# Performance work log

Measured on AMD Instinct MI355X. Metric: run time of the kernel, lower is better.

## Reference

```python
import jax, jax.numpy as jnp
import numpy as np

N = 100000   # nodes
E = 1600000  # edges
IN, HID, OUT = 128, 128, 64
K = 32       # MaxK top-k
NUM_LAYERS = 2


def _xavier(key, shape):
    lim = float(np.sqrt(6.0 / (shape[0] + shape[1])))
    return jax.random.uniform(key, shape, jnp.float32, -lim, lim)


def setup_inputs() -> dict:
    key = jax.random.key(0)
    ks = jax.random.split(key, 8)
    return {
        "x": jax.random.normal(ks[0], (N, IN), jnp.float32),
        "src": jax.random.randint(ks[1], (E,), 0, N, dtype=jnp.int32),
        "dst": jax.random.randint(ks[2], (E,), 0, N, dtype=jnp.int32),
        "W_in": _xavier(ks[3], (IN, HID)), "b_in": jnp.zeros((HID,), jnp.float32),
        "W1": _xavier(ks[4], (HID, HID)), "b1": jnp.zeros((HID,), jnp.float32),
        "bg1": jnp.zeros((HID,), jnp.float32),
        "W2": _xavier(ks[5], (HID, HID)), "b2": jnp.zeros((HID,), jnp.float32),
        "bg2": jnp.zeros((HID,), jnp.float32),
        "W_out": _xavier(ks[6], (HID, OUT)), "b_out": jnp.zeros((OUT,), jnp.float32),
    }


def _maxk(x, k):
    # keep top-k entries per row, zero the rest (straight-through mask)
    _, idx = jax.lax.top_k(x, k)                      # [N, k]
    rows = jnp.arange(x.shape[0])[:, None]
    mask = jnp.zeros_like(x).at[rows, idx].set(1.0)
    return x * mask


def _graph_conv(x, src, dst, bias):
    # DGL GraphConv, norm='both', weight=None: D_dst^{-1/2} A D_src^{-1/2} x + b
    ones = jnp.ones((src.shape[0],), x.dtype)
    deg_out = jnp.maximum(jax.ops.segment_sum(ones, src, num_segments=N), 1.0)
    deg_in = jnp.maximum(jax.ops.segment_sum(ones, dst, num_segments=N), 1.0)
    msg = (x * (deg_out ** -0.5)[:, None])[src]        # [E, HID] gather
    agg = jax.ops.segment_sum(msg, dst, num_segments=N)  # [N, HID] scatter-add
    return agg * (deg_in ** -0.5)[:, None] + bias


def reference(x, src, dst, W_in, b_in, W1, b1, bg1, W2, b2, bg2, W_out, b_out):
    h = jax.nn.relu(x @ W_in + b_in)
    for W, b, bg in ((W1, b1, bg1), (W2, b2, bg2)):
        h = h @ W + b
        h = _maxk(h, K)
        # dropout: eval-mode identity
        h = _graph_conv(h, src, dst, bg)
    return h @ W_out + b_out
```

## Files before the change

kernel.cpp:

```cpp
#include <hip/hip_runtime.h>

#define NN   100000
#define EE   1600000
#define HIDF 128
#define OUTF 64
#define KSEL 32
#define BSH  3
#define NBK  (NN >> BSH)
#define CAPSH 8
#define CAP  (1 << CAPSH)

static __device__ __forceinline__ unsigned int sortable_key(float f) {
    unsigned int u = __float_as_uint(f);
    return (u & 0x80000000u) ? ~u : (u | 0x80000000u);
}

__global__ __launch_bounds__(256) void bin_fill(const int* __restrict__ src,
                                                const int* __restrict__ dst,
                                                int* __restrict__ bcnt,
                                                int* __restrict__ scnt,
                                                int2* __restrict__ bin, int e) {
    int i = blockIdx.x * 256 + threadIdx.x;
    if (i < e) {
        int s = src[i];
        int d = dst[i];
        int b = d >> BSH;
        int pos = atomicAdd(&bcnt[b], 1);
        if (pos < CAP) bin[((size_t)b << CAPSH) + pos] = make_int2(s, d);
        atomicAdd(&scnt[s], 1);
    }
}

__global__ __launch_bounds__(128) void csr_from_bin(const int2* __restrict__ bin,
                                                    const int* __restrict__ bcnt,
                                                    int* __restrict__ row_off,
                                                    int* __restrict__ cnt_in,
                                                    float* __restrict__ dvin,
                                                    int* __restrict__ csr, int n) {
    __shared__ int cnt8[1 << BSH];
    __shared__ int cur8[1 << BSH];
    const int b = blockIdx.x;
    const int t = threadIdx.x;
    if (t < (1 << BSH)) cnt8[t] = 0;
    __syncthreads();
    const int m = min(bcnt[b], CAP);
    const size_t base = (size_t)b << CAPSH;
    for (int e = t; e < m; e += 128) {
        atomicAdd(&cnt8[bin[base + e].y & ((1 << BSH) - 1)], 1);
    }
    __syncthreads();
    if (t < (1 << BSH)) {
        int pre = 0;
#pragma unroll
        for (int q = 0; q < (1 << BSH); ++q) pre += (q < t) ? cnt8[q] : 0;
        int node = (b << BSH) + t;
        int start = (int)base + pre;
        if (node < n) {
            row_off[node] = start;
            cnt_in[node] = cnt8[t];
            dvin[node] = rsqrtf((float)max(cnt8[t], 1));
        }
        cur8[t] = start;
    }
    __syncthreads();
    for (int e = t; e < m; e += 128) {
        int2 r = bin[base + e];
        int pos = atomicAdd(&cur8[r.y & ((1 << BSH) - 1)], 1);
        csr[pos] = r.x;
    }
}

__global__ __launch_bounds__(256) void dvout_pass(const int* __restrict__ scnt,
                                                  float* __restrict__ dvo, int n) {
    int i = blockIdx.x * 256 + threadIdx.x;
    if (i < n) dvo[i] = rsqrtf((float)max(scnt[i], 1));
}

__global__ __launch_bounds__(256, 2) void gemm_relu(const float* __restrict__ A,
                                                    const float* __restrict__ W,
                                                    const float* __restrict__ bias,
                                                    float* __restrict__ out, int n) {
    __shared__ float As[64][128];
    __shared__ float Ws[16][128];
    const int tid = threadIdx.x;
    const int rbase = blockIdx.x * 64;
    const int cc = tid & 31;
    const int r0 = (tid >> 5) * 8;
    float acc[8][4];
#pragma unroll
    for (int i = 0; i < 8; ++i) { acc[i][0] = 0.f; acc[i][1] = 0.f; acc[i][2] = 0.f; acc[i][3] = 0.f; }

    float4 wreg0 = *(const float4*)(W + (size_t)tid * 4);
    float4 wreg1 = *(const float4*)(W + (size_t)(tid + 256) * 4);

#pragma unroll
    for (int q = 0; q < 8; ++q) {
        int f = q * 256 + tid;
        int row = rbase + (f >> 5);
        float4 v = make_float4(0.f, 0.f, 0.f, 0.f);
        if (row < n) v = *(const float4*)(A + (size_t)row * 128 + (f & 31) * 4);
        *(float4*)&As[f >> 5][(f & 31) * 4] = v;
    }

    for (int p = 0; p < 8; ++p) {
        const int kb = p * 16;
        if (p) __syncthreads();
        *(float4*)&Ws[tid >> 5][(tid & 31) * 4] = wreg0;
        *(float4*)&Ws[(tid >> 5) + 8][(tid & 31) * 4] = wreg1;
        if (p < 7) {
            const float* wp = W + (size_t)(kb + 16) * 128;
            wreg0 = *(const float4*)(wp + (size_t)tid * 4);
            wreg1 = *(const float4*)(wp + (size_t)(tid + 256) * 4);
        }
        __syncthreads();
#pragma unroll
        for (int kq = 0; kq < 4; ++kq) {
            int k = kq * 4;
            float4 w0 = *(float4*)&Ws[k + 0][cc * 4];
            float4 w1 = *(float4*)&Ws[k + 1][cc * 4];
            float4 w2 = *(float4*)&Ws[k + 2][cc * 4];
            float4 w3 = *(float4*)&Ws[k + 3][cc * 4];
#pragma unroll
            for (int i = 0; i < 8; ++i) {
                float4 a = *(float4*)&As[r0 + i][kb + k];
                acc[i][0] += a.x * w0.x + a.y * w1.x + a.z * w2.x + a.w * w3.x;
                acc[i][1] += a.x * w0.y + a.y * w1.y + a.z * w2.y + a.w * w3.y;
                acc[i][2] += a.x * w0.z + a.y * w1.z + a.z * w2.z + a.w * w3.z;
                acc[i][3] += a.x * w0.w + a.y * w1.w + a.z * w2.w + a.w * w3.w;
            }
        }
    }
    float4 b4 = *(const float4*)(bias + cc * 4);
#pragma unroll
    for (int i = 0; i < 8; ++i) {
        int gr = rbase + r0 + i;
        if (gr < n) {
            float4 o = make_float4(fmaxf(acc[i][0] + b4.x, 0.f), fmaxf(acc[i][1] + b4.y, 0.f),
                                   fmaxf(acc[i][2] + b4.z, 0.f), fmaxf(acc[i][3] + b4.w, 0.f));
            *(float4*)(out + (size_t)gr * 128 + cc * 4) = o;
        }
    }
}

__global__ __launch_bounds__(256, 2) void gemm_maxk(const float* __restrict__ A,
                                                    const float* __restrict__ W,
                                                    const float* __restrict__ bias,
                                                    const float* __restrict__ dvout,
                                                    float* __restrict__ svals, int n) {
    __shared__ float As[64][128];
    __shared__ float Ws[16][128];
    const int tid = threadIdx.x;
    const int rbase = blockIdx.x * 64;
    const int cc = tid & 31;
    const int r0 = (tid >> 5) * 8;
    float acc[8][4];
#pragma unroll
    for (int i = 0; i < 8; ++i) { acc[i][0] = 0.f; acc[i][1] = 0.f; acc[i][2] = 0.f; acc[i][3] = 0.f; }

    float4 wreg0 = *(const float4*)(W + (size_t)tid * 4);
    float4 wreg1 = *(const float4*)(W + (size_t)(tid + 256) * 4);

#pragma unroll
    for (int q = 0; q < 8; ++q) {
        int f = q * 256 + tid;
        *(float4*)&As[f >> 5][(f & 31) * 4] =
            *(const float4*)(A + (size_t)rbase * 128 + (size_t)f * 4);
    }

    for (int p = 0; p < 8; ++p) {
        const int kb = p * 16;
        if (p) __syncthreads();
        *(float4*)&Ws[tid >> 5][(tid & 31) * 4] = wreg0;
        *(float4*)&Ws[(tid >> 5) + 8][(tid & 31) * 4] = wreg1;
        if (p < 7) {
            const float* wp = W + (size_t)(kb + 16) * 128;
            wreg0 = *(const float4*)(wp + (size_t)tid * 4);
            wreg1 = *(const float4*)(wp + (size_t)(tid + 256) * 4);
        }
        __syncthreads();
#pragma unroll
        for (int kq = 0; kq < 4; ++kq) {
            int k = kq * 4;
            float4 w0 = *(float4*)&Ws[k + 0][cc * 4];
            float4 w1 = *(float4*)&Ws[k + 1][cc * 4];
            float4 w2 = *(float4*)&Ws[k + 2][cc * 4];
            float4 w3 = *(float4*)&Ws[k + 3][cc * 4];
#pragma unroll
            for (int i = 0; i < 8; ++i) {
                float4 a = *(float4*)&As[r0 + i][kb + k];
                acc[i][0] += a.x * w0.x + a.y * w1.x + a.z * w2.x + a.w * w3.x;
                acc[i][1] += a.x * w0.y + a.y * w1.y + a.z * w2.y + a.w * w3.y;
                acc[i][2] += a.x * w0.z + a.y * w1.z + a.z * w2.z + a.w * w3.z;
                acc[i][3] += a.x * w0.w + a.y * w1.w + a.z * w2.w + a.w * w3.w;
            }
        }
    }

    const int lane = tid & 63;
    const int wvi = tid >> 6;
    const bool up = lane >= 32;
    const unsigned lt32 = (1u << (lane & 31)) - 1u;
    float4 b4 = *(const float4*)(bias + cc * 4);

    unsigned keys[8][4];
#pragma unroll
    for (int i = 0; i < 8; ++i) {
        acc[i][0] += b4.x; acc[i][1] += b4.y; acc[i][2] += b4.z; acc[i][3] += b4.w;
        keys[i][0] = sortable_key(acc[i][0]);
        keys[i][1] = sortable_key(acc[i][1]);
        keys[i][2] = sortable_key(acc[i][2]);
        keys[i][3] = sortable_key(acc[i][3]);
    }
    unsigned prefL[8], prefU[8];
#pragma unroll
    for (int i = 0; i < 8; ++i) { prefL[i] = 0u; prefU[i] = 0u; }

    for (int bit = 31; bit >= 8; --bit) {
        unsigned msk = 1u << bit;
#pragma unroll
        for (int i = 0; i < 8; ++i) {
            unsigned cL = prefL[i] | msk;
            unsigned cU = prefU[i] | msk;
            unsigned myc = up ? cU : cL;
            unsigned long long b0 = __ballot(keys[i][0] >= myc);
            unsigned long long b1 = __ballot(keys[i][1] >= myc);
            unsigned long long b2 = __ballot(keys[i][2] >= myc);
            unsigned long long b3 = __ballot(keys[i][3] >= myc);
            int cntL = __popc((unsigned)b0) + __popc((unsigned)b1) +
                       __popc((unsigned)b2) + __popc((unsigned)b3);
            int cntU = __popc((unsigned)(b0 >> 32)) + __popc((unsigned)(b1 >> 32)) +
                       __popc((unsigned)(b2 >> 32)) + __popc((unsigned)(b3 >> 32));
            prefL[i] = (cntL >= KSEL) ? cL : prefL[i];
            prefU[i] = (cntU >= KSEL) ? cU : prefU[i];
        }
    }

#pragma unroll 1
    for (int i = 0; i < 8; ++i) {
        int row = rbase + 16 * wvi + i + (up ? 8 : 0);
        unsigned myp = up ? prefU[i] : prefL[i];
        unsigned kb0 = keys[i][0] & 0xFFFFFF00u, kb1 = keys[i][1] & 0xFFFFFF00u;
        unsigned kb2 = keys[i][2] & 0xFFFFFF00u, kb3 = keys[i][3] & 0xFFFFFF00u;
        unsigned long long g0 = __ballot(kb0 > myp), g1 = __ballot(kb1 > myp);
        unsigned long long g2 = __ballot(kb2 > myp), g3 = __ballot(kb3 > myp);
        unsigned long long e0 = __ballot(kb0 == myp), e1 = __ballot(kb1 == myp);
        unsigned long long e2 = __ballot(kb2 == myp), e3 = __ballot(kb3 == myp);
        unsigned gh0 = up ? (unsigned)(g0 >> 32) : (unsigned)g0;
        unsigned gh1 = up ? (unsigned)(g1 >> 32) : (unsigned)g1;
        unsigned gh2 = up ? (unsigned)(g2 >> 32) : (unsigned)g2;
        unsigned gh3 = up ? (unsigned)(g3 >> 32) : (unsigned)g3;
        unsigned eh0 = up ? (unsigned)(e0 >> 32) : (unsigned)e0;
        unsigned eh1 = up ? (unsigned)(e1 >> 32) : (unsigned)e1;
        unsigned eh2 = up ? (unsigned)(e2 >> 32) : (unsigned)e2;
        unsigned eh3 = up ? (unsigned)(e3 >> 32) : (unsigned)e3;
        int m = __popc(gh0) + __popc(gh1) + __popc(gh2) + __popc(gh3);
        int need = KSEL - m;
        int gpos = __popc(gh0 & lt32) + __popc(gh1 & lt32) + __popc(gh2 & lt32) + __popc(gh3 & lt32);
        int epos = __popc(eh0 & lt32) + __popc(eh1 & lt32) + __popc(eh2 & lt32) + __popc(eh3 & lt32);
        bool ok = row < n;
        float ds = dvout[row];
        size_t base = (size_t)row * 32;
        unsigned cbit = (unsigned)(lane & 31);
        {
            int slot = -1;
            if (kb0 > myp) slot = gpos;
            else if (kb0 == myp && epos < need) slot = m + epos;
            if (slot >= 0 && ok) {
                unsigned u = (__float_as_uint(acc[i][0] * ds) & 0xFFFFFF80u) | (unsigned)(cc * 4 + 0);
                svals[base + slot] = __uint_as_float(u);
            }
            gpos += (gh0 >> cbit) & 1u;
            epos += (eh0 >> cbit) & 1u;
        }
        {
            int slot = -1;
            if (kb1 > myp) slot = gpos;
            else if (kb1 == myp && epos < need) slot = m + epos;
            if (slot >= 0 && ok) {
                unsigned u = (__float_as_uint(acc[i][1] * ds) & 0xFFFFFF80u) | (unsigned)(cc * 4 + 1);
                svals[base + slot] = __uint_as_float(u);
            }
            gpos += (gh1 >> cbit) & 1u;
            epos += (eh1 >> cbit) & 1u;
        }
        {
            int slot = -1;
            if (kb2 > myp) slot = gpos;
            else if (kb2 == myp && epos < need) slot = m + epos;
            if (slot >= 0 && ok) {
                unsigned u = (__float_as_uint(acc[i][2] * ds) & 0xFFFFFF80u) | (unsigned)(cc * 4 + 2);
                svals[base + slot] = __uint_as_float(u);
            }
            gpos += (gh2 >> cbit) & 1u;
            epos += (eh2 >> cbit) & 1u;
        }
        {
            int slot = -1;
            if (kb3 > myp) slot = gpos;
            else if (kb3 == myp && epos < need) slot = m + epos;
            if (slot >= 0 && ok) {
                unsigned u = (__float_as_uint(acc[i][3] * ds) & 0xFFFFFF80u) | (unsigned)(cc * 4 + 3);
                svals[base + slot] = __uint_as_float(u);
            }
        }
    }
}

__global__ __launch_bounds__(256) void agg_kernel(const float* __restrict__ svals,
                                                  const int* __restrict__ row_off,
                                                  const int* __restrict__ cnt_in,
                                                  const int* __restrict__ csr_src,
                                                  const float* __restrict__ dvin,
                                                  const float* __restrict__ bg,
                                                  float* __restrict__ out, int n) {
    __shared__ float acc[4][2][128];
    const int wv = threadIdx.x >> 6;
    const int lane = threadIdx.x & 63;
    const int sub = lane >> 5;
    const int j = lane & 31;
    const int node = blockIdx.x * 4 + wv;
    float* base0 = &acc[wv][0][0];
    base0[lane] = 0.f;
    base0[lane + 64] = 0.f;
    base0[lane + 128] = 0.f;
    base0[lane + 192] = 0.f;
    if (node < n) {
        int s0 = row_off[node], s1 = s0 + cnt_in[node];
        float* Ac = &acc[wv][sub][0];
        int e = s0 + sub;
        for (; e + 2 < s1; e += 4) {
            int sA = csr_src[e];
            int sB = csr_src[e + 2];
            float vA = svals[(size_t)sA * 32 + j];
            float vB = svals[(size_t)sB * 32 + j];
            int fA = (int)(__float_as_uint(vA) & 127u);
            Ac[fA] += vA;
            int fB = (int)(__float_as_uint(vB) & 127u);
            Ac[fB] += vB;
        }
        for (; e < s1; e += 2) {
            int sA = csr_src[e];
            float vA = svals[(size_t)sA * 32 + j];
            int fA = (int)(__float_as_uint(vA) & 127u);
            Ac[fA] += vA;
        }
    }
    if (node < n) {
        float dv = dvin[node];
        float r0 = acc[wv][0][lane] + acc[wv][1][lane];
        float r1 = acc[wv][0][lane + 64] + acc[wv][1][lane + 64];
        out[(size_t)node * 128 + lane] = r0 * dv + bg[lane];
        out[(size_t)node * 128 + lane + 64] = r1 * dv + bg[lane + 64];
    }
}

__global__ __launch_bounds__(256, 2) void gemm_out64(const float* __restrict__ A,
                                                     const float* __restrict__ W,
                                                     const float* __restrict__ bias,
                                                     float* __restrict__ out, int n) {
    __shared__ float As[64][128];
    __shared__ float Ws[32][64];
    const int tid = threadIdx.x;
    const int rbase = blockIdx.x * 64;
    const int cc = tid & 15;
    const int r0 = (tid >> 4) * 4;
    float acc[4][4];
#pragma unroll
    for (int i = 0; i < 4; ++i) { acc[i][0] = 0.f; acc[i][1] = 0.f; acc[i][2] = 0.f; acc[i][3] = 0.f; }

    float4 wreg0 = *(const float4*)(W + (size_t)tid * 4);
    float4 wreg1 = *(const float4*)(W + (size_t)(tid + 256) * 4);

#pragma unroll
    for (int q = 0; q < 8; ++q) {
        int f = q * 256 + tid;
        *(float4*)&As[f >> 5][(f & 31) * 4] =
            *(const float4*)(A + (size_t)rbase * 128 + (size_t)f * 4);
    }

    for (int p = 0; p < 4; ++p) {
        const int kb = p * 32;
        if (p) __syncthreads();
        *(float4*)&Ws[tid >> 4][(tid & 15) * 4] = wreg0;
        *(float4*)&Ws[(tid >> 4) + 16][(tid & 15) * 4] = wreg1;
        if (p < 3) {
            const float* wp = W + (size_t)(kb + 32) * 64;
            wreg0 = *(const float4*)(wp + (size_t)tid * 4);
            wreg1 = *(const float4*)(wp + (size_t)(tid + 256) * 4);
        }
        __syncthreads();
#pragma unroll
        for (int kq = 0; kq < 8; ++kq) {
            int k = kq * 4;
            float4 w0 = *(float4*)&Ws[k + 0][cc * 4];
            float4 w1 = *(float4*)&Ws[k + 1][cc * 4];
            float4 w2 = *(float4*)&Ws[k + 2][cc * 4];
            float4 w3 = *(float4*)&Ws[k + 3][cc * 4];
#pragma unroll
            for (int i = 0; i < 4; ++i) {
                float4 a = *(float4*)&As[r0 + i][kb + k];
                acc[i][0] += a.x * w0.x + a.y * w1.x + a.z * w2.x + a.w * w3.x;
                acc[i][1] += a.x * w0.y + a.y * w1.y + a.z * w2.y + a.w * w3.y;
                acc[i][2] += a.x * w0.z + a.y * w1.z + a.z * w2.z + a.w * w3.z;
                acc[i][3] += a.x * w0.w + a.y * w1.w + a.z * w2.w + a.w * w3.w;
            }
        }
    }
    float4 b4 = *(const float4*)(bias + cc * 4);
#pragma unroll
    for (int i = 0; i < 4; ++i) {
        int gr = rbase + r0 + i;
        if (gr < n) {
            float4 o = make_float4(acc[i][0] + b4.x, acc[i][1] + b4.y,
                                   acc[i][2] + b4.z, acc[i][3] + b4.w);
            *(float4*)(out + (size_t)gr * 64 + cc * 4) = o;
        }
    }
}

extern "C" void kernel_launch(void* const* d_in, const int* in_sizes, int n_in,
                              void* d_out, int out_size, void* d_ws, size_t ws_size,
                              hipStream_t stream) {
    const float* x     = (const float*)d_in[0];
    const int*   src   = (const int*)d_in[1];
    const int*   dst   = (const int*)d_in[2];
    const float* W_in  = (const float*)d_in[3];
    const float* b_in  = (const float*)d_in[4];
    const float* W1    = (const float*)d_in[5];
    const float* b1    = (const float*)d_in[6];
    const float* bg1   = (const float*)d_in[7];
    const float* W2    = (const float*)d_in[8];
    const float* b2    = (const float*)d_in[9];
    const float* bg2   = (const float*)d_in[10];
    const float* W_out = (const float*)d_in[11];
    const float* b_out = (const float*)d_in[12];
    float* out = (float*)d_out;

    char* p = (char*)d_ws;
    auto carve = [&](size_t bytes) {
        char* r = p;
        p += (bytes + 255) & ~(size_t)255;
        return r;
    };
    int*   scnt    = (int*)carve((size_t)NN * 4);
    int*   bcnt    = (int*)carve((size_t)NBK * 4);
    float* dvout   = (float*)carve((size_t)(NN + 128) * 4);
    float* dvin    = (float*)carve((size_t)NN * 4);
    int*   row_off = (int*)carve((size_t)NN * 4);
    int*   cnt_in  = (int*)carve((size_t)NN * 4);
    int*   csr_src = (int*)carve((size_t)NBK * CAP * 4);
    float* hbuf    = (float*)carve((size_t)(NN + 128) * HIDF * 4);
    float* svals   = (float*)carve((size_t)NN * KSEL * 4);

    int2* bin = (int2*)hbuf;

    const int gN   = (NN + 255) / 256;
    const int gE   = (EE + 255) / 256;
    const int gT   = (NN + 63) / 64;
    const int gAgg = (NN + 3) / 4;

    hipMemsetAsync(scnt, 0, (size_t)NN * 4, stream);
    hipMemsetAsync(bcnt, 0, (size_t)NBK * 4, stream);
    bin_fill<<<gE, 256, 0, stream>>>(src, dst, bcnt, scnt, bin, EE);
    csr_from_bin<<<NBK, 128, 0, stream>>>(bin, bcnt, row_off, cnt_in, dvin, csr_src, NN);
    dvout_pass<<<gN, 256, 0, stream>>>(scnt, dvout, NN);

    gemm_relu<<<gT, 256, 0, stream>>>(x, W_in, b_in, hbuf, NN);

    gemm_maxk<<<gT, 256, 0, stream>>>(hbuf, W1, b1, dvout, svals, NN);
    agg_kernel<<<gAgg, 256, 0, stream>>>(svals, row_off, cnt_in, csr_src, dvin, bg1, hbuf, NN);

    gemm_maxk<<<gT, 256, 0, stream>>>(hbuf, W2, b2, dvout, svals, NN);
    agg_kernel<<<gAgg, 256, 0, stream>>>(svals, row_off, cnt_in, csr_src, dvin, bg2, hbuf, NN);

    gemm_out64<<<gT, 256, 0, stream>>>(hbuf, W_out, b_out, out, NN);
}
```

Before: 700.2 us.

## Fuse graph preprocessing into GEMM launches via heterogeneous block roles

Merges the edge-binning pass with the input ReLU GEMM, and the CSR build with the first MaxK GEMM, into single launches where blocks take different roles by block index. This lets the independent graph preprocessing and dense work share the GPU and removes launch gaps. The separate dvout kernel is dropped and out-degree normalization is computed inline from source counts. Bin entries are packed into one int each (src shifted, dst low bits) and moved to a dedicated buffer so they no longer alias hbuf. The risks are extra register and LDS pressure from the shared kernel bodies, and a silent overflow in the packed encoding if node ids ever grew too large.

```diff
diff --git a/kernel.cpp b/kernel.cpp
--- a/kernel.cpp
+++ b/kernel.cpp
@@ -9,83 +9,44 @@
 #define NBK  (NN >> BSH)
 #define CAPSH 8
 #define CAP  (1 << CAPSH)
+#define GT   ((NN + 63) / 64)
+#define GE   ((EE + 255) / 256)
 
 static __device__ __forceinline__ unsigned int sortable_key(float f) {
     unsigned int u = __float_as_uint(f);
     return (u & 0x80000000u) ? ~u : (u | 0x80000000u);
 }
 
-__global__ __launch_bounds__(256) void bin_fill(const int* __restrict__ src,
-                                                const int* __restrict__ dst,
-                                                int* __restrict__ bcnt,
-                                                int* __restrict__ scnt,
-                                                int2* __restrict__ bin, int e) {
-    int i = blockIdx.x * 256 + threadIdx.x;
-    if (i < e) {
-        int s = src[i];
-        int d = dst[i];
-        int b = d >> BSH;
-        int pos = atomicAdd(&bcnt[b], 1);
-        if (pos < CAP) bin[((size_t)b << CAPSH) + pos] = make_int2(s, d);
-        atomicAdd(&scnt[s], 1);
-    }
-}
-
-__global__ __launch_bounds__(128) void csr_from_bin(const int2* __restrict__ bin,
-                                                    const int* __restrict__ bcnt,
-                                                    int* __restrict__ row_off,
-                                                    int* __restrict__ cnt_in,
-                                                    float* __restrict__ dvin,
-                                                    int* __restrict__ csr, int n) {
-    __shared__ int cnt8[1 << BSH];
-    __shared__ int cur8[1 << BSH];
-    const int b = blockIdx.x;
-    const int t = threadIdx.x;
-    if (t < (1 << BSH)) cnt8[t] = 0;
-    __syncthreads();
-    const int m = min(bcnt[b], CAP);
-    const size_t base = (size_t)b << CAPSH;
-    for (int e = t; e < m; e += 128) {
-        atomicAdd(&cnt8[bin[base + e].y & ((1 << BSH) - 1)], 1);
-    }
-    __syncthreads();
-    if (t < (1 << BSH)) {
-        int pre = 0;
-#pragma unroll
-        for (int q = 0; q < (1 << BSH); ++q) pre += (q < t) ? cnt8[q] : 0;
-        int node = (b << BSH) + t;
-        int start = (int)base + pre;
-        if (node < n) {
-            row_off[node] = start;
-            cnt_in[node] = cnt8[t];
-            dvin[node] = rsqrtf((float)max(cnt8[t], 1));
-        }
-        cur8[t] = start;
-    }
-    __syncthreads();
-    for (int e = t; e < m; e += 128) {
-        int2 r = bin[base + e];
-        int pos = atomicAdd(&cur8[r.y & ((1 << BSH) - 1)], 1);
-        csr[pos] = r.x;
-    }
-}
-
-__global__ __launch_bounds__(256) void dvout_pass(const int* __restrict__ scnt,
-                                                  float* __restrict__ dvo, int n) {
-    int i = blockIdx.x * 256 + threadIdx.x;
-    if (i < n) dvo[i] = rsqrtf((float)max(scnt[i], 1));
-}
-
-__global__ __launch_bounds__(256, 2) void gemm_relu(const float* __restrict__ A,
-                                                    const float* __restrict__ W,
-                                                    const float* __restrict__ bias,
-                                                    float* __restrict__ out, int n) {
+__global__ __launch_bounds__(256, 2) void fused_bin_relu(const int* __restrict__ src,
+                                                         const int* __restrict__ dst,
+                                                         int* __restrict__ bcnt,
+                                                         int* __restrict__ scnt,
+                                                         int* __restrict__ bin,
+                                                         const float* __restrict__ X,
+                                                         const float* __restrict__ W,
+                                                         const float* __restrict__ bias,
+                                                         float* __restrict__ out) {
     __shared__ float As[64][128];
     __shared__ float Ws[16][128];
     const int tid = threadIdx.x;
-    const int rbase = blockIdx.x * 64;
+
+    if (blockIdx.x < GE) {
+        int i = blockIdx.x * 256 + tid;
+        if (i < EE) {
+            int s = src[i];
+            int d = dst[i];
+            int b = d >> BSH;
+            int pos = atomicAdd(&bcnt[b], 1);
+            if (pos < CAP) bin[(b << CAPSH) + pos] = (s << BSH) | (d & ((1 << BSH) - 1));
+            atomicAdd(&scnt[s], 1);
+        }
+        return;
+    }
+
+    const int rbase = (blockIdx.x - GE) * 64;
     const int cc = tid & 31;
     const int r0 = (tid >> 5) * 8;
+    const int n = NN;
     float acc[8][4];
 #pragma unroll
     for (int i = 0; i < 8; ++i) { acc[i][0] = 0.f; acc[i][1] = 0.f; acc[i][2] = 0.f; acc[i][3] = 0.f; }
@@ -98,7 +59,7 @@
         int f = q * 256 + tid;
         int row = rbase + (f >> 5);
         float4 v = make_float4(0.f, 0.f, 0.f, 0.f);
-        if (row < n) v = *(const float4*)(A + (size_t)row * 128 + (f & 31) * 4);
+        if (row < n) v = *(const float4*)(X + (size_t)row * 128 + (f & 31) * 4);
         *(float4*)&As[f >> 5][(f & 31) * 4] = v;
     }
 
@@ -142,15 +103,14 @@
     }
 }
 
-__global__ __launch_bounds__(256, 2) void gemm_maxk(const float* __restrict__ A,
-                                                    const float* __restrict__ W,
-                                                    const float* __restrict__ bias,
-                                                    const float* __restrict__ dvout,
-                                                    float* __restrict__ svals, int n) {
-    __shared__ float As[64][128];
-    __shared__ float Ws[16][128];
+static __device__ __forceinline__ void gemm_maxk_body(float (*As)[128], float (*Ws)[128],
+                                                      const float* __restrict__ A,
+                                                      const float* __restrict__ W,
+                                                      const float* __restrict__ bias,
+                                                      const int* __restrict__ scnt,
+                                                      float* __restrict__ svals,
+                                                      int n, int rbase) {
     const int tid = threadIdx.x;
-    const int rbase = blockIdx.x * 64;
     const int cc = tid & 31;
     const int r0 = (tid >> 5) * 8;
     float acc[8][4];
@@ -258,7 +218,8 @@
         int gpos = __popc(gh0 & lt32) + __popc(gh1 & lt32) + __popc(gh2 & lt32) + __popc(gh3 & lt32);
         int epos = __popc(eh0 & lt32) + __popc(eh1 & lt32) + __popc(eh2 & lt32) + __popc(eh3 & lt32);
         bool ok = row < n;
-        float ds = dvout[row];
+        float ds = 0.f;
+        if (ok) ds = rsqrtf((float)max(scnt[row], 1));
         size_t base = (size_t)row * 32;
         unsigned cbit = (unsigned)(lane & 31);
         {
@@ -304,6 +265,68 @@
             }
         }
     }
+}
+
+__global__ __launch_bounds__(256, 2) void fused_csr_maxk(const int* __restrict__ bin,
+                                                         const int* __restrict__ bcnt,
+                                                         int* __restrict__ row_off,
+                                                         int* __restrict__ cnt_in,
+                                                         float* __restrict__ dvin,
+                                                         int* __restrict__ csr,
+                                                         const float* __restrict__ A,
+                                                         const float* __restrict__ W,
+                                                         const float* __restrict__ bias,
+                                                         const int* __restrict__ scnt,
+                                                         float* __restrict__ svals) {
+    __shared__ float As[64][128];
+    __shared__ float Ws[16][128];
+    const int tid = threadIdx.x;
+
+    if (blockIdx.x >= GT) {
+        int* cnt8 = (int*)&As[0][0];
+        int* cur8 = cnt8 + (1 << BSH);
+        const int b = blockIdx.x - GT;
+        if (tid < (1 << BSH)) cnt8[tid] = 0;
+        __syncthreads();
+        const int m = min(bcnt[b], CAP);
+        const int base = b << CAPSH;
+        for (int e = tid; e < m; e += 256) {
+            atomicAdd(&cnt8[bin[base + e] & ((1 << BSH) - 1)], 1);
+        }
+        __syncthreads();
+        if (tid < (1 << BSH)) {
+            int pre = 0;
+#pragma unroll
+            for (int q = 0; q < (1 << BSH); ++q) pre += (q < tid) ? cnt8[q] : 0;
+            int node = (b << BSH) + tid;
+            int start = base + pre;
+            if (node < NN) {
+                row_off[node] = start;
+                cnt_in[node] = cnt8[tid];
+                dvin[node] = rsqrtf((float)max(cnt8[tid], 1));
+            }
+            cur8[tid] = start;
+        }
+        __syncthreads();
+        for (int e = tid; e < m; e += 256) {
+            int r = bin[base + e];
+            int pos = atomicAdd(&cur8[r & ((1 << BSH) - 1)], 1);
+            csr[pos] = r >> BSH;
+        }
+        return;
+    }
+
+    gemm_maxk_body(As, Ws, A, W, bias, scnt, svals, NN, blockIdx.x * 64);
+}
+
+__global__ __launch_bounds__(256, 2) void gemm_maxk(const float* __restrict__ A,
+                                                    const float* __restrict__ W,
+                                                    const float* __restrict__ bias,
+                                                    const int* __restrict__ scnt,
+                                                    float* __restrict__ svals, int n) {
+    __shared__ float As[64][128];
+    __shared__ float Ws[16][128];
+    gemm_maxk_body(As, Ws, A, W, bias, scnt, svals, n, blockIdx.x * 64);
 }
 
 __global__ __launch_bounds__(256) void agg_kernel(const float* __restrict__ svals,
@@ -444,34 +467,27 @@
     };
     int*   scnt    = (int*)carve((size_t)NN * 4);
     int*   bcnt    = (int*)carve((size_t)NBK * 4);
-    float* dvout   = (float*)carve((size_t)(NN + 128) * 4);
     float* dvin    = (float*)carve((size_t)NN * 4);
     int*   row_off = (int*)carve((size_t)NN * 4);
     int*   cnt_in  = (int*)carve((size_t)NN * 4);
+    int*   bin     = (int*)carve((size_t)NBK * CAP * 4);
     int*   csr_src = (int*)carve((size_t)NBK * CAP * 4);
     float* hbuf    = (float*)carve((size_t)(NN + 128) * HIDF * 4);
     float* svals   = (float*)carve((size_t)NN * KSEL * 4);
 
-    int2* bin = (int2*)hbuf;
-
-    const int gN   = (NN + 255) / 256;
-    const int gE   = (EE + 255) / 256;
-    const int gT   = (NN + 63) / 64;
     const int gAgg = (NN + 3) / 4;
 
     hipMemsetAsync(scnt, 0, (size_t)NN * 4, stream);
     hipMemsetAsync(bcnt, 0, (size_t)NBK * 4, stream);
-    bin_fill<<<gE, 256, 0, stream>>>(src, dst, bcnt, scnt, bin, EE);
-    csr_from_bin<<<NBK, 128, 0, stream>>>(bin, bcnt, row_off, cnt_in, dvin, csr_src, NN);
-    dvout_pass<<<gN, 256, 0, stream>>>(scnt, dvout, NN);
-
-    gemm_relu<<<gT, 256, 0, stream>>>(x, W_in, b_in, hbuf, NN);
-
-    gemm_maxk<<<gT, 256, 0, stream>>>(hbuf, W1, b1, dvout, svals, NN);
+
+    fused_bin_relu<<<GE + GT, 256, 0, stream>>>(src, dst, bcnt, scnt, bin,
+                                                x, W_in, b_in, hbuf);
+    fused_csr_maxk<<<GT + NBK, 256, 0, stream>>>(bin, bcnt, row_off, cnt_in, dvin, csr_src,
+                                                 hbuf, W1, b1, scnt, svals);
     agg_kernel<<<gAgg, 256, 0, stream>>>(svals, row_off, cnt_in, csr_src, dvin, bg1, hbuf, NN);
 
-    gemm_maxk<<<gT, 256, 0, stream>>>(hbuf, W2, b2, dvout, svals, NN);
+    gemm_maxk<<<GT, 256, 0, stream>>>(hbuf, W2, b2, scnt, svals, NN);
     agg_kernel<<<gAgg, 256, 0, stream>>>(svals, row_off, cnt_in, csr_src, dvin, bg2, hbuf, NN);
 
-    gemm_out64<<<gT, 256, 0, stream>>>(hbuf, W_out, b_out, out, NN);
-}
+    gemm_out64<<<GT, 256, 0, stream>>>(hbuf, W_out, b_out, out, NN);
+}
```

New measurement: 683.3 us. -2.4%, faster.
